# Performance work log

Measured on AMD Instinct MI355X. Metric: run time of the kernel, lower is better.

The kernel has to match this reference:

```python
import jax, jax.numpy as jnp
import numpy as np
from jax.scipy.ndimage import map_coordinates

IMG = 256
N_ANG = 50
BATCH = 4
N_CNN = 32
IN_CH = 2


def _circle_mask(S):
    c = (S - 1) / 2.0
    yy, xx = jnp.meshgrid(jnp.arange(S, dtype=jnp.float32), jnp.arange(S, dtype=jnp.float32), indexing='ij')
    return (((yy - c) ** 2 + (xx - c) ** 2) <= (S / 2.0) ** 2).astype(jnp.float32)


def radon_forward(img, angles):
    # img [B,1,S,S] -> sinogram [B,1,A,S]; parallel-beam, clip_to_circle=True
    S = img.shape[-1]
    c = (S - 1) / 2.0
    img = img * _circle_mask(S)
    t = jnp.arange(S, dtype=jnp.float32) - c        # integration coord
    s = jnp.arange(S, dtype=jnp.float32) - c        # detector coord
    cos = jnp.cos(angles)[:, None, None]
    sin = jnp.sin(angles)[:, None, None]
    x = s[None, None, :] * cos - t[None, :, None] * sin   # [A,S,S]
    y = s[None, None, :] * sin + t[None, :, None] * cos
    coords = jnp.stack([y + c, x + c])                    # [2,A,S,S] (row, col)
    samp = jax.vmap(lambda im: map_coordinates(im, coords, order=1, mode='constant', cval=0.0))(img[:, 0])  # [B,A,S,S]
    return samp.sum(axis=2)[:, None]                      # sum over ray param -> [B,1,A,S]


def filter_sinogram(sino):
    # Ram-Lak FFT filter with zero-padding + FBP normalization
    S = sino.shape[-1]
    A = sino.shape[2]
    P = max(64, int(2 ** np.ceil(np.log2(2 * S))))
    f = jnp.fft.rfft(jnp.pad(sino, ((0, 0), (0, 0), (0, 0), (0, P - S))), axis=-1)
    ramp = 2.0 * jnp.fft.rfftfreq(P).astype(jnp.float32)
    out = jnp.fft.irfft(f * ramp, n=P, axis=-1)[..., :S]
    return out * (np.pi / (2.0 * A))


def radon_backprojection(sino, angles):
    # sino [B,1,A,S] -> image [B,1,S,S]
    B, _, A, S = sino.shape
    c = (S - 1) / 2.0
    yy, xx = jnp.meshgrid(jnp.arange(S, dtype=jnp.float32) - c, jnp.arange(S, dtype=jnp.float32) - c, indexing='ij')
    cos = jnp.cos(angles)[:, None, None]
    sin = jnp.sin(angles)[:, None, None]
    det = xx[None] * cos + yy[None] * sin + c             # [A,S,S] detector coord
    sino2 = sino[:, 0]                                    # [B,A,S]

    def interp_one(sino_a, idx):
        # sino_a [B,S], idx [S,S] -> [B,S,S] linear interp, zero outside
        i0 = jnp.clip(jnp.floor(idx).astype(jnp.int32), 0, S - 2)
        w = idx - i0
        v = sino_a[:, i0] * (1.0 - w) + sino_a[:, i0 + 1] * w
        valid = (idx >= 0.0) & (idx <= S - 1.0)
        return jnp.where(valid, v, 0.0)

    bp = jax.vmap(interp_one, in_axes=(1, 0))(sino2, det).sum(axis=0)  # [B,S,S]
    return (bp * _circle_mask(S))[:, None]


def conv2d(x, w, b):
    y = jax.lax.conv_general_dilated(x, w, (1, 1), 'SAME', dimension_numbers=('NCHW', 'OIHW', 'NCHW'))
    return y + b[None, :, None, None]


def setup_inputs() -> dict:
    key = jax.random.key(0)
    ks = jax.random.split(key, 10)
    angles = jnp.asarray(np.linspace(0, np.pi, N_ANG, endpoint=False), dtype=jnp.float32)
    return {
        'x_sinogram': jax.random.normal(ks[0], (BATCH, 1, N_ANG, IMG), dtype=jnp.float32),
        'y_img_prev': jax.random.normal(ks[1], (BATCH, 1, IMG, IMG), dtype=jnp.float32),
        'y_img_concat_prev': jax.random.normal(ks[2], (BATCH, 1, IMG, IMG), dtype=jnp.float32),
        'angles': angles,
        'step': jnp.float32(1.0),
        'w1': jax.random.normal(ks[3], (N_CNN, IN_CH, 3, 3), dtype=jnp.float32) * 0.1,
        'b1': jnp.zeros((N_CNN,), dtype=jnp.float32),
        'w2': jax.random.normal(ks[4], (N_CNN, N_CNN, 3, 3), dtype=jnp.float32) * 0.1,
        'b2': jnp.zeros((N_CNN,), dtype=jnp.float32),
        'w3': jax.random.normal(ks[5], (1, N_CNN, 3, 3), dtype=jnp.float32) * 0.1,
        'b3': jnp.zeros((1,), dtype=jnp.float32),
    }


def reference(x_sinogram, y_img_prev, y_img_concat_prev, angles, step, w1, b1, w2, b2, w3, b3):
    Ay = radon_forward(y_img_prev, angles)                 # [B,1,A,S]
    diff = Ay - x_sinogram
    filt = filter_sinogram(diff)
    fbp = radon_backprojection(filt, angles)               # [B,1,S,S]
    y_img_update = y_img_prev + step * fbp
    y_cat = jnp.concatenate([y_img_update, y_img_concat_prev], axis=1)  # [B,2,S,S]
    h = jax.nn.relu(conv2d(y_cat, w1, b1))
    h = jax.nn.relu(conv2d(h, w2, b2))
    y_img = conv2d(h, w3, b3)
    return (y_img, y_img_update)
```

## Files before the change

kernel.cpp:

```cpp
#include <hip/hip_runtime.h>
#include <math.h>

#define IMGS 256
#define NANG 50
#define BATCH 4
#define NCNN 32
#define PIX (IMGS*IMGS)
#define NPIX (BATCH*PIX)

#define OFF_FILT  0
#define OFF_W2BF  51200

static constexpr double PI_D = 3.14159265358979323846;

typedef unsigned short u16;
typedef unsigned int   u32;
typedef unsigned long long u64;
typedef __bf16 bfrag __attribute__((ext_vector_type(8)));
typedef float  ffrag __attribute__((ext_vector_type(4)));

__device__ __forceinline__ u16 f2bf(float f) {
    u32 u = __float_as_uint(f);
    u += 0x7fffu + ((u >> 16) & 1u);
    return (u16)(u >> 16);
}

#define RPITCH_D 131
__global__ __launch_bounds__(1024, 4) void k_A(const float* __restrict__ angles,
                                               const float* __restrict__ yprev,
                                               const float* __restrict__ xsino,
                                               const float* __restrict__ w2,
                                               float* __restrict__ ws) {
    __shared__ u16 limg[258 * 262];
    __shared__ float spart[1024];
    __shared__ float staps[512];
    __shared__ float srow[256];
    int tid = threadIdx.x;
    int gid = blockIdx.x;
    if (gid >= 200) {
        int i = (gid - 200) * 1024 + tid;
        if (i < 9216) {
            int t = i >> 10, oc = (i >> 5) & 31, ic = i & 31;
            ((u16*)(ws + OFF_W2BF))[i] = f2bf(w2[(oc * 32 + ic) * 9 + t]);
        }
        return;
    }
    u32* l32 = (u32*)limg;
    int ra = gid;
    int a = ra % NANG, b = ra / NANG;

    if (tid < 511) {
        int d = tid - 255;
        int n = d < 0 ? -d : d;
        double g;
        if (n == 0) {
            g = 0.5;
        } else {
            double th = PI_D * (double)n / 256.0;
            double S = (256.0 * cos(255.0 * th) - 255.0 * cos(256.0 * th) - 1.0)
                       / (2.0 * (1.0 - cos(th)));
            double sign = (n & 1) ? -1.0 : 1.0;
            g = (sign + S / 128.0) / 512.0;
        }
        staps[tid] = (float)(g * PI_D / 100.0);
    }

    for (int z = tid; z < 772; z += 1024) {
        int addr;
        if (z < 258)      addr = z * RPITCH_D;
        else if (z < 516) addr = (z - 258) * RPITCH_D + 129;
        else if (z < 644) addr = (z - 516) + 1;
        else              addr = 257 * RPITCH_D + (z - 644) + 1;
        l32[addr] = 0;
    }
    const float* __restrict__ src = yprev + b * PIX;
    for (int idx = tid; idx < 16384; idx += 1024) {
        int r = idx >> 6, c4 = (idx & 63) << 2;
        float4 v = *(const float4*)(src + r * 256 + c4);
        float di = (float)r - 127.5f;
        float rr = di * di;
        float d0 = (float)c4 - 127.5f;
        v.x = (rr + d0 * d0 <= 16384.0f) ? v.x : 0.0f;
        v.y = (rr + (d0 + 1.0f) * (d0 + 1.0f) <= 16384.0f) ? v.y : 0.0f;
        v.z = (rr + (d0 + 2.0f) * (d0 + 2.0f) <= 16384.0f) ? v.z : 0.0f;
        v.w = (rr + (d0 + 3.0f) * (d0 + 3.0f) <= 16384.0f) ? v.w : 0.0f;
        u32 p0 = (u32)f2bf(v.x) | ((u32)f2bf(v.y) << 16);
        u32 p1 = (u32)f2bf(v.z) | ((u32)f2bf(v.w) << 16);
        int dw = (r + 1) * RPITCH_D + (c4 >> 1) + 1;
        l32[dw] = p0; l32[dw + 1] = p1;
    }
    __syncthreads();

    float a_ = angles[a];
    float cs = cosf(a_), sn = sinf(a_);
    int lane = tid & 63, w = tid >> 6;
    int s8 = lane & 7, t8 = lane >> 3;
    int sA = w * 16 + s8;
    float scA = (float)sA - 127.5f;

    float loA = (float)(w * 16) - 127.5f, hiA = loA + 7.0f;
    float loB = loA + 8.0f,               hiB = hiA + 8.0f;
    float s2minA = fminf(loA * loA, hiA * hiA);
    float s2maxA = fmaxf(loA * loA, hiA * hiA);
    float s2minB = fminf(loB * loB, hiB * hiB);
    float s2maxB = fmaxf(loB * loB, hiB * hiB);
    float s2min  = fminf(s2minA, s2minB);
    float s2max  = fmaxf(s2maxA, s2maxB);
    float hmax = sqrtf(16770.25f - s2min);
    int j_lo = max(0, (int)ceilf((120.5f - hmax) * 0.125f));
    int j_hi = min(31, (int)floorf((127.5f + hmax) * 0.125f));

    float tc0 = (float)t8 - 127.5f + 8.0f * (float)j_lo;
    float rowA = scA * sn + tc0 * cs + 127.5f;
    float colA = scA * cs - tc0 * sn + 127.5f;
    float rowB = rowA + 8.0f * sn;
    float colB = colA + 8.0f * cs;
    float cs8 = 8.0f * cs, sn8 = 8.0f * sn;
    float accA = 0.0f, accB = 0.0f;
    #pragma unroll 2
    for (int j = j_lo; j <= j_hi; ++j) {
        float t0j = 8.0f * (float)j - 127.5f;
        float t7j = t0j + 7.0f;
        float tmax2 = fmaxf(t0j * t0j, t7j * t7j);
        if (s2max + tmax2 <= 16384.0f) {
            #pragma unroll
            for (int hh = 0; hh < 2; ++hh) {
                float rowv = hh ? rowB : rowA;
                float colv = hh ? colB : colA;
                float fr = floorf(rowv), fc = floorf(colv);
                float wr = rowv - fr, wc = colv - fc;
                int i0 = (int)fr, j0 = (int)fc;
                int ca = j0 + 2;
                int ka = ca >> 1;
                int sh = (ca & 1) << 4;
                int dw = (i0 + 1) * RPITCH_D + ka;
                u32 A = l32[dw],            C = l32[dw + 1];
                u32 B = l32[dw + RPITCH_D], D = l32[dw + RPITCH_D + 1];
                u32 top = (u32)((((u64)C << 32) | (u64)A) >> sh);
                u32 bot = (u32)((((u64)D << 32) | (u64)B) >> sh);
                float tl = __uint_as_float(top << 16);
                float tr_ = __uint_as_float(top & 0xffff0000u);
                float bl = __uint_as_float(bot << 16);
                float br = __uint_as_float(bot & 0xffff0000u);
                float tv = tl + (tr_ - tl) * wc;
                float bv = bl + (br - bl) * wc;
                float sv = tv + (bv - tv) * wr;
                if (hh) accB += sv; else accA += sv;
            }
        } else {
            #pragma unroll
            for (int hh = 0; hh < 2; ++hh) {
                float rowv = hh ? rowB : rowA;
                float colv = hh ? colB : colA;
                float fr = floorf(rowv), fc = floorf(colv);
                float wr = rowv - fr, wc = colv - fc;
                int i0 = (int)fr, j0 = (int)fc;
                bool valid = (rowv > -1.0f) & (rowv < 256.0f) & (colv > -1.0f) & (colv < 256.0f);
                int i0c = min(max(i0, -1), 255);
                int j0c = min(max(j0, -1), 255);
                int ca = j0c + 2;
                int ka = ca >> 1;
                int sh = (ca & 1) << 4;
                int dw = (i0c + 1) * RPITCH_D + ka;
                u32 A = l32[dw],            C = l32[dw + 1];
                u32 B = l32[dw + RPITCH_D], D = l32[dw + RPITCH_D + 1];
                u32 top = (u32)((((u64)C << 32) | (u64)A) >> sh);
                u32 bot = (u32)((((u64)D << 32) | (u64)B) >> sh);
                float tl = __uint_as_float(top << 16);
                float tr_ = __uint_as_float(top & 0xffff0000u);
                float bl = __uint_as_float(bot << 16);
                float br = __uint_as_float(bot & 0xffff0000u);
                float tv = tl + (tr_ - tl) * wc;
                float bv = bl + (br - bl) * wc;
                float sv = tv + (bv - tv) * wr;
                sv = valid ? sv : 0.0f;
                if (hh) accB += sv; else accA += sv;
            }
        }
        rowA += cs8; colA -= sn8; rowB += cs8; colB -= sn8;
    }
    accA += __shfl_xor(accA, 8, 64);
    accA += __shfl_xor(accA, 16, 64);
    accA += __shfl_xor(accA, 32, 64);
    accB += __shfl_xor(accB, 8, 64);
    accB += __shfl_xor(accB, 16, 64);
    accB += __shfl_xor(accB, 32, 64);
    if (t8 == 0) { spart[sA] = accA; spart[sA + 8] = accB; }
    __syncthreads();
    if (tid < 256)
        srow[tid] = spart[tid] - xsino[ra * 256 + tid];
    __syncthreads();
    {
        int s = tid & 255, q = tid >> 8;
        float fa = 0.0f;
        int m0 = q * 64;
        #pragma unroll 8
        for (int m = m0; m < m0 + 64; ++m) fa += srow[m] * staps[s - m + 255];
        spart[tid] = fa;
    }
    __syncthreads();
    if (tid < 256)
        ws[OFF_FILT + ra * 256 + tid] =
            spart[tid] + spart[tid + 256] + spart[tid + 512] + spart[tid + 768];
}

#define H2PITCH 36
#define SM_SF    0
#define SM_H1    0
#define SM_H2    51200
#define SM_SUPD  125504
#define SM_SY2   133824
#define SM_SCS   142144
#define SM_SSN   142344
#define SM_SWP   142544
#define SM_TOTAL 143120
#define H1QSTRIDE (6*130*8)

__global__ __launch_bounds__(512, 2) void k_BC(const float* __restrict__ angles,
                                               const float* __restrict__ yprev,
                                               const float* __restrict__ yconc,
                                               const float* __restrict__ stepp,
                                               const float* __restrict__ w1,
                                               const float* __restrict__ b1,
                                               const float* __restrict__ b2,
                                               const float* __restrict__ w3,
                                               const float* __restrict__ b3,
                                               float* __restrict__ ws,
                                               float* __restrict__ dout) {
    __shared__ __align__(16) unsigned char smem[SM_TOTAL];
    float* sf   = (float*)(smem + SM_SF);
    u16*   h1q  = (u16*)(smem + SM_H1);
    u16*   sh2  = (u16*)(smem + SM_H2);
    u32*   l32c = (u32*)(smem + SM_H2);
    float (*supd)[260] = (float(*)[260])(smem + SM_SUPD);
    float (*sy2)[260]  = (float(*)[260])(smem + SM_SY2);
    float* scs = (float*)(smem + SM_SCS);
    float* ssn = (float*)(smem + SM_SSN);
    u32*   swp = (u32*)(smem + SM_SWP);

    int tid = threadIdx.x;
    int b = blockIdx.x >> 7, tile = blockIdx.x & 127;
    int y0 = tile << 1;

    {
        const float4* s4 = (const float4*)(ws + OFF_FILT + b * (NANG * 256));
        float4* d4 = (float4*)sf;
        for (int idx = tid; idx < NANG * 64; idx += 512) d4[idx] = s4[idx];
    }
    if (tid < NANG) {
        float a_ = angles[tid];
        scs[tid] = cosf(a_); ssn[tid] = sinf(a_);
    }
    if (tid < 144) {
        int t = tid >> 4, kd = tid & 15;
        swp[tid] = (u32)f2bf(w3[(2 * kd) * 9 + t]) | ((u32)f2bf(w3[(2 * kd + 1) * 9 + t]) << 16);
    }
    if (tid < 32) {
        int r = tid >> 2, c4 = tid & 3;
        supd[r][(c4 < 2) ? c4 : (c4 + 256)] = 0.0f;
    }
    for (int idx = tid; idx < 8 * 260; idx += 512) {
        int r = idx / 260, c = idx - r * 260;
        int iy = y0 - 3 + r, ix = c - 2;
        sy2[r][c] = ((unsigned)iy < 256u && (unsigned)ix < 256u)
                        ? yconc[b * PIX + iy * 256 + ix] : 0.0f;
    }
    __syncthreads();

    {
        int j = tid & 255, r0 = tid >> 8;
        float xx = (float)j - 127.5f;
        float yyb = (float)(y0 - 3 + r0) - 127.5f;
        float ac0 = 0.f, ac1 = 0.f, ac2 = 0.f, ac3 = 0.f;
        #pragma unroll 2
        for (int a = 0; a < NANG; ++a) {
            float cs = scs[a], sn = ssn[a];
            float d2 = sn + sn;
            float f0 = xx * cs + yyb * sn + 127.5f;
            float f1 = f0 + d2, f2 = f1 + d2, f3 = f2 + d2;
            #define BPSAMP(ff, accv) { \
                float fl = floorf(ff); int i0 = (int)fl; \
                i0 = min(max(i0, 0), 254); \
                float wq = ff - (float)i0; \
                float v = sf[a * 256 + i0] * (1.0f - wq) + sf[a * 256 + i0 + 1] * wq; \
                accv += (ff >= 0.0f && ff <= 255.0f) ? v : 0.0f; }
            BPSAMP(f0, ac0) BPSAMP(f1, ac1) BPSAMP(f2, ac2) BPSAMP(f3, ac3)
            #undef BPSAMP
        }
        float step = stepp[0];
        float accs[4] = {ac0, ac1, ac2, ac3};
        #pragma unroll
        for (int k = 0; k < 4; ++k) {
            int lr = r0 + 2 * k;
            int iy = y0 - 3 + lr;
            float val = 0.0f;
            if ((unsigned)iy < 256u) {
                float yy = (float)iy - 127.5f;
                float mk = (xx * xx + yy * yy <= 16384.0f) ? 1.0f : 0.0f;
                val = yprev[b * PIX + iy * 256 + j] + step * accs[k] * mk;
                if (iy >= y0 && iy <= y0 + 1)
                    dout[NPIX + b * PIX + iy * 256 + j] = val;
            }
            supd[lr][j + 2] = val;
        }
    }
    __syncthreads();

    if (tid < 144) {
        int r = tid / 36, rem = tid % 36;
        int col = (rem < 18) ? 0 : 257, dw = rem % 18;
        l32c[(r * 258 + col) * 18 + dw] = 0;
    }
    #pragma unroll
    for (int r = 0; r < 4; ++r) {
        int hy = y0 - 1 + r;
        if (hy < 0 || hy > 255)
            for (int idx = tid; idx < 258 * 18; idx += 512)
                l32c[r * 258 * 18 + idx] = 0;
    }

    const u16* __restrict__ w2bf = (const u16*)(ws + OFF_W2BF);
    int wv = tid >> 6, lane = tid & 63;
    int m = lane & 15, quad = lane >> 4;
    bfrag Bf[9][2];
    #pragma unroll
    for (int t = 0; t < 9; ++t) {
        const u16* wp = w2bf + t * 1024 + m * 32 + quad * 8;
        Bf[t][0] = *(const bfrag*)(wp);
        Bf[t][1] = *(const bfrag*)(wp + 16 * 32);
    }
    float bias0 = b2[m], bias1 = b2[m + 16];

    for (int xh = 0; xh < 2; ++xh) {
        {
            int oc0 = wv * 4, qq = wv >> 1, hh = wv & 1;
            float W[72];
            const float4* wsrc = (const float4*)(w1 + oc0 * 18);
            #pragma unroll
            for (int i = 0; i < 18; ++i) ((float4*)W)[i] = wsrc[i];
            float bb0 = b1[oc0], bb1 = b1[oc0 + 1], bb2 = b1[oc0 + 2], bb3 = b1[oc0 + 3];
            u16* hq = h1q + qq * H1QSTRIDE + hh * 4;
            for (int it = 0; it < 7; ++it) {
                int idx = it * 64 + lane;
                if (idx < 390) {
                    int lr = idx / 65, pp = idx - lr * 65;
                    int ir = y0 - 2 + lr;
                    int P = xh * 128 + 2 * pp - 1;
                    int cb = P + 1 + 2 - xh * 256;
                    int cgb = P + 1;
                    float a00 = bb0, a01 = bb1, a02 = bb2, a03 = bb3;
                    float a10 = bb0, a11 = bb1, a12 = bb2, a13 = bb3;
                    #pragma unroll
                    for (int ky = 0; ky < 3; ++ky) {
                        float2 ua = *(const float2*)&supd[lr + ky][cgb];
                        float2 ub = *(const float2*)&supd[lr + ky][cgb + 2];
                        float2 ca = *(const float2*)&sy2[lr + ky][cgb];
                        float2 cb2 = *(const float2*)&sy2[lr + ky][cgb + 2];
                        float u[4]  = {ua.x, ua.y, ub.x, ub.y};
                        float c6[4] = {ca.x, ca.y, cb2.x, cb2.y};
                        #pragma unroll
                        for (int kx = 0; kx < 3; ++kx) {
                            int t = ky * 3 + kx;
                            float u0 = u[kx],     c0 = c6[kx];
                            float u1 = u[kx + 1], c1 = c6[kx + 1];
                            a00 += u0 * W[t]      + c0 * W[9 + t];
                            a01 += u0 * W[18 + t] + c0 * W[27 + t];
                            a02 += u0 * W[36 + t] + c0 * W[45 + t];
                            a03 += u0 * W[54 + t] + c0 * W[63 + t];
                            a10 += u1 * W[t]      + c1 * W[9 + t];
                            a11 += u1 * W[18 + t] + c1 * W[27 + t];
                            a12 += u1 * W[36 + t] + c1 * W[45 + t];
                            a13 += u1 * W[54 + t] + c1 * W[63 + t];
                        }
                    }
                    bool rowOK = (unsigned)ir < 256u;
                    bool v0 = rowOK && ((unsigned)P < 256u);
                    bool v1 = rowOK && ((unsigned)(P + 1) < 256u);
                    u32 q00 = 0, q01 = 0, q10 = 0, q11 = 0;
                    if (v0) {
                        q00 = (u32)f2bf(fmaxf(a00, 0.f)) | ((u32)f2bf(fmaxf(a01, 0.f)) << 16);
                        q01 = (u32)f2bf(fmaxf(a02, 0.f)) | ((u32)f2bf(fmaxf(a03, 0.f)) << 16);
                    }
                    if (v1) {
                        q10 = (u32)f2bf(fmaxf(a10, 0.f)) | ((u32)f2bf(fmaxf(a11, 0.f)) << 16);
                        q11 = (u32)f2bf(fmaxf(a12, 0.f)) | ((u32)f2bf(fmaxf(a13, 0.f)) << 16);
                    }
                    int cl = 2 * pp;
                    u32* op0 = (u32*)(hq + (lr * 130 + cl) * 8);
                    u32* op1 = (u32*)(hq + (lr * 130 + cl + 1) * 8);
                    op0[0] = q00; op0[1] = q01;
                    op1[0] = q10; op1[1] = q11;
                }
            }
        }
        __syncthreads();

        {
            const u16* Abase = h1q + quad * H1QSTRIDE;
            #pragma unroll
            for (int k = 0; k < 4; ++k) {
                int tl = wv + (k << 3);
                int ridx = tl >> 3, xt8 = tl & 7;
                int hy = y0 - 1 + ridx;
                bool valid = (unsigned)hy < 256u;
                int clb = (xt8 << 4) + m;
                bfrag A0[3], A1[3];
                #pragma unroll
                for (int tx = 0; tx < 3; ++tx)
                    A0[tx] = *(const bfrag*)(Abase + ((ridx + 0) * 130 + clb + tx) * 8);
                #pragma unroll
                for (int tx = 0; tx < 3; ++tx)
                    A1[tx] = *(const bfrag*)(Abase + ((ridx + 1) * 130 + clb + tx) * 8);
                ffrag c0 = {0.f, 0.f, 0.f, 0.f}, c1 = {0.f, 0.f, 0.f, 0.f};
                #pragma unroll
                for (int tx = 0; tx < 3; ++tx) {
                    c0 = __builtin_amdgcn_mfma_f32_16x16x32_bf16(A0[tx], Bf[tx][0], c0, 0, 0, 0);
                    c1 = __builtin_amdgcn_mfma_f32_16x16x32_bf16(A0[tx], Bf[tx][1], c1, 0, 0, 0);
                }
                #pragma unroll
                for (int tx = 0; tx < 3; ++tx)
                    A0[tx] = *(const bfrag*)(Abase + ((ridx + 2) * 130 + clb + tx) * 8);
                #pragma unroll
                for (int tx = 0; tx < 3; ++tx) {
                    c0 = __builtin_amdgcn_mfma_f32_16x16x32_bf16(A1[tx], Bf[3 + tx][0], c0, 0, 0, 0);
                    c1 = __builtin_amdgcn_mfma_f32_16x16x32_bf16(A1[tx], Bf[3 + tx][1], c1, 0, 0, 0);
                }
                #pragma unroll
                for (int tx = 0; tx < 3; ++tx) {
                    c0 = __builtin_amdgcn_mfma_f32_16x16x32_bf16(A0[tx], Bf[6 + tx][0], c0, 0, 0, 0);
                    c1 = __builtin_amdgcn_mfma_f32_16x16x32_bf16(A0[tx], Bf[6 + tx][1], c1, 0, 0, 0);
                }
                if (valid) {
                    #pragma unroll
                    for (int r = 0; r < 4; ++r) {
                        int px = xh * 128 + (xt8 << 4) + quad * 4 + r;
                        u16* op = sh2 + (ridx * 258 + px + 1) * H2PITCH;
                        op[m]      = f2bf(fmaxf(c0[r] + bias0, 0.0f));
                        op[m + 16] = f2bf(fmaxf(c1[r] + bias1, 0.0f));
                    }
                }
            }
        }
        __syncthreads();
    }

    {
        int rr = tid >> 8, x = tid & 255;
        int oy = y0 + rr;
        float acc = b3[0];
        #pragma unroll
        for (int ky = 0; ky < 3; ++ky) {
            #pragma unroll
            for (int cx = 0; cx < 3; ++cx) {
                int t = ky * 3 + cx;
                const uint2* q2 = (const uint2*)(l32c + ((rr + ky) * 258 + x + cx) * 18);
                const uint2* w2p = (const uint2*)(swp + t * 16);
                #pragma unroll
                for (int kd = 0; kd < 8; ++kd) {
                    uint2 hv = q2[kd];
                    uint2 wvv = w2p[kd];
                    acc += __uint_as_float(hv.x << 16) * __uint_as_float(wvv.x << 16)
                         + __uint_as_float(hv.x & 0xffff0000u) * __uint_as_float(wvv.x & 0xffff0000u)
                         + __uint_as_float(hv.y << 16) * __uint_as_float(wvv.y << 16)
                         + __uint_as_float(hv.y & 0xffff0000u) * __uint_as_float(wvv.y & 0xffff0000u);
                }
            }
        }
        dout[b * PIX + oy * 256 + x] = acc;
    }
}

extern "C" void kernel_launch(void* const* d_in, const int* in_sizes, int n_in,
                              void* d_out, int out_size, void* d_ws, size_t ws_size,
                              hipStream_t stream) {
    const float* xsino  = (const float*)d_in[0];
    const float* yprev  = (const float*)d_in[1];
    const float* yconc  = (const float*)d_in[2];
    const float* angles = (const float*)d_in[3];
    const float* stepp  = (const float*)d_in[4];
    const float* w1 = (const float*)d_in[5];
    const float* b1 = (const float*)d_in[6];
    const float* w2 = (const float*)d_in[7];
    const float* b2 = (const float*)d_in[8];
    const float* w3 = (const float*)d_in[9];
    const float* b3 = (const float*)d_in[10];
    float* out = (float*)d_out;
    float* ws  = (float*)d_ws;

    k_A<<<209, 1024, 0, stream>>>(angles, yprev, xsino, w2, ws);
    k_BC<<<BATCH * 128, 512, 0, stream>>>(angles, yprev, yconc, stepp, w1, b1,
                                          b2, w3, b3, ws, out);
}
```

Baseline: 175.8 us.

## Split fused conv stage into four column quarters to halve shared memory

```diff
diff --git a/kernel.cpp b/kernel.cpp
--- a/kernel.cpp
+++ b/kernel.cpp
@@ -204,19 +204,20 @@
             spart[tid] + spart[tid + 256] + spart[tid + 512] + spart[tid + 768];
 }
 
+#define H1COLS 82
+#define H1PLANE (6*H1COLS*4)
+#define H2COLS 80
 #define H2PITCH 36
-#define SM_SF    0
 #define SM_H1    0
-#define SM_H2    51200
-#define SM_SUPD  125504
-#define SM_SY2   133824
-#define SM_SCS   142144
-#define SM_SSN   142344
-#define SM_SWP   142544
-#define SM_TOTAL 143120
-#define H1QSTRIDE (6*130*8)
-
-__global__ __launch_bounds__(512, 2) void k_BC(const float* __restrict__ angles,
+#define SM_H2    31488
+#define SM_SUPD  54528
+#define SM_SY2   62848
+#define SM_SCS   71168
+#define SM_SSN   71368
+#define SM_SWP   71568
+#define SM_TOTAL 72192
+
+__global__ __launch_bounds__(512, 4) void k_BC(const float* __restrict__ angles,
                                                const float* __restrict__ yprev,
                                                const float* __restrict__ yconc,
                                                const float* __restrict__ stepp,
@@ -228,10 +229,10 @@
                                                float* __restrict__ ws,
                                                float* __restrict__ dout) {
     __shared__ __align__(16) unsigned char smem[SM_TOTAL];
-    float* sf   = (float*)(smem + SM_SF);
-    u16*   h1q  = (u16*)(smem + SM_H1);
+    float* sf   = (float*)(smem);
+    u16*   h1   = (u16*)(smem + SM_H1);
     u16*   sh2  = (u16*)(smem + SM_H2);
-    u32*   l32c = (u32*)(smem + SM_H2);
+    u32*   l32h2= (u32*)(smem + SM_H2);
     float (*supd)[260] = (float(*)[260])(smem + SM_SUPD);
     float (*sy2)[260]  = (float(*)[260])(smem + SM_SY2);
     float* scs = (float*)(smem + SM_SCS);
@@ -306,48 +307,30 @@
     }
     __syncthreads();
 
-    if (tid < 144) {
-        int r = tid / 36, rem = tid % 36;
-        int col = (rem < 18) ? 0 : 257, dw = rem % 18;
-        l32c[(r * 258 + col) * 18 + dw] = 0;
-    }
-    #pragma unroll
-    for (int r = 0; r < 4; ++r) {
-        int hy = y0 - 1 + r;
-        if (hy < 0 || hy > 255)
-            for (int idx = tid; idx < 258 * 18; idx += 512)
-                l32c[r * 258 * 18 + idx] = 0;
-    }
-
-    const u16* __restrict__ w2bf = (const u16*)(ws + OFF_W2BF);
     int wv = tid >> 6, lane = tid & 63;
     int m = lane & 15, quad = lane >> 4;
-    bfrag Bf[9][2];
-    #pragma unroll
-    for (int t = 0; t < 9; ++t) {
-        const u16* wp = w2bf + t * 1024 + m * 32 + quad * 8;
-        Bf[t][0] = *(const bfrag*)(wp);
-        Bf[t][1] = *(const bfrag*)(wp + 16 * 32);
-    }
     float bias0 = b2[m], bias1 = b2[m + 16];
-
-    for (int xh = 0; xh < 2; ++xh) {
+    const u16* __restrict__ w2bf = (const u16*)(ws + OFF_W2BF);
+
+    for (int xq = 0; xq < 4; ++xq) {
+        int xbase = xq * 64;
         {
-            int oc0 = wv * 4, qq = wv >> 1, hh = wv & 1;
+            int oc0 = wv * 4;
             float W[72];
             const float4* wsrc = (const float4*)(w1 + oc0 * 18);
             #pragma unroll
             for (int i = 0; i < 18; ++i) ((float4*)W)[i] = wsrc[i];
             float bb0 = b1[oc0], bb1 = b1[oc0 + 1], bb2 = b1[oc0 + 2], bb3 = b1[oc0 + 3];
-            u16* hq = h1q + qq * H1QSTRIDE + hh * 4;
-            for (int it = 0; it < 7; ++it) {
+            u16* hp = h1 + wv * H1PLANE;
+            #pragma unroll
+            for (int it = 0; it < 4; ++it) {
                 int idx = it * 64 + lane;
-                if (idx < 390) {
-                    int lr = idx / 65, pp = idx - lr * 65;
+                if (idx < 246) {
+                    int lr = idx / 41, pp = idx - lr * 41;
+                    int P = xbase - 9 + 2 * pp;
                     int ir = y0 - 2 + lr;
-                    int P = xh * 128 + 2 * pp - 1;
-                    int cb = P + 1 + 2 - xh * 256;
                     int cgb = P + 1;
+                    cgb = min(max(cgb, 0), 256);
                     float a00 = bb0, a01 = bb1, a02 = bb2, a03 = bb3;
                     float a10 = bb0, a11 = bb1, a12 = bb2, a13 = bb3;
                     #pragma unroll
@@ -385,88 +368,105 @@
                         q10 = (u32)f2bf(fmaxf(a10, 0.f)) | ((u32)f2bf(fmaxf(a11, 0.f)) << 16);
                         q11 = (u32)f2bf(fmaxf(a12, 0.f)) | ((u32)f2bf(fmaxf(a13, 0.f)) << 16);
                     }
-                    int cl = 2 * pp;
-                    u32* op0 = (u32*)(hq + (lr * 130 + cl) * 8);
-                    u32* op1 = (u32*)(hq + (lr * 130 + cl + 1) * 8);
-                    op0[0] = q00; op0[1] = q01;
-                    op1[0] = q10; op1[1] = q11;
+                    uint4* op = (uint4*)(hp + (lr * H1COLS + 2 * pp) * 4);
+                    *op = make_uint4(q00, q01, q10, q11);
                 }
             }
         }
         __syncthreads();
 
         {
-            const u16* Abase = h1q + quad * H1QSTRIDE;
-            #pragma unroll
-            for (int k = 0; k < 4; ++k) {
+            bfrag Bf[9][2];
+            #pragma unroll
+            for (int t = 0; t < 9; ++t) {
+                const u16* wp = w2bf + t * 1024 + m * 32 + quad * 8;
+                Bf[t][0] = *(const bfrag*)(wp);
+                Bf[t][1] = *(const bfrag*)(wp + 16 * 32);
+            }
+            #pragma unroll
+            for (int k = 0; k < 3; ++k) {
                 int tl = wv + (k << 3);
-                int ridx = tl >> 3, xt8 = tl & 7;
-                int hy = y0 - 1 + ridx;
-                bool valid = (unsigned)hy < 256u;
-                int clb = (xt8 << 4) + m;
-                bfrag A0[3], A1[3];
+                if (tl < 20) {
+                    int ridx = tl / 5, pt = tl - ridx * 5;
+                    int hy = y0 - 1 + ridx;
+                    bool hyOK = (unsigned)hy < 256u;
+                    int Lb = 16 * pt + m;
+                    const u16* qp = h1 + quad * (2 * H1PLANE);
+                    #define LDF(row, L, dst) { \
+                        const u16* p0_ = qp + ((row) * H1COLS + (L)) * 4; \
+                        uint2 lo_ = *(const uint2*)p0_; \
+                        uint2 hi_ = *(const uint2*)(p0_ + H1PLANE); \
+                        ((uint2*)&dst)[0] = lo_; ((uint2*)&dst)[1] = hi_; }
+                    bfrag A0[3], A1[3];
+                    #pragma unroll
+                    for (int tx = 0; tx < 3; ++tx) LDF(ridx + 0, Lb + tx, A0[tx])
+                    #pragma unroll
+                    for (int tx = 0; tx < 3; ++tx) LDF(ridx + 1, Lb + tx, A1[tx])
+                    ffrag c0 = {0.f, 0.f, 0.f, 0.f}, c1 = {0.f, 0.f, 0.f, 0.f};
+                    #pragma unroll
+                    for (int tx = 0; tx < 3; ++tx) {
+                        c0 = __builtin_amdgcn_mfma_f32_16x16x32_bf16(A0[tx], Bf[tx][0], c0, 0, 0, 0);
+                        c1 = __builtin_amdgcn_mfma_f32_16x16x32_bf16(A0[tx], Bf[tx][1], c1, 0, 0, 0);
+                    }
+                    #pragma unroll
+                    for (int tx = 0; tx < 3; ++tx) LDF(ridx + 2, Lb + tx, A0[tx])
+                    #pragma unroll
+                    for (int tx = 0; tx < 3; ++tx) {
+                        c0 = __builtin_amdgcn_mfma_f32_16x16x32_bf16(A1[tx], Bf[3 + tx][0], c0, 0, 0, 0);
+                        c1 = __builtin_amdgcn_mfma_f32_16x16x32_bf16(A1[tx], Bf[3 + tx][1], c1, 0, 0, 0);
+                    }
+                    #pragma unroll
+                    for (int tx = 0; tx < 3; ++tx) {
+                        c0 = __builtin_amdgcn_mfma_f32_16x16x32_bf16(A0[tx], Bf[6 + tx][0], c0, 0, 0, 0);
+                        c1 = __builtin_amdgcn_mfma_f32_16x16x32_bf16(A0[tx], Bf[6 + tx][1], c1, 0, 0, 0);
+                    }
+                    #undef LDF
+                    #pragma unroll
+                    for (int r = 0; r < 4; ++r) {
+                        int pl = 16 * pt + quad * 4 + r;
+                        int pimg = xbase - 8 + pl;
+                        bool ok = hyOK && ((unsigned)pimg < 256u);
+                        float f0 = ok ? fmaxf(c0[r] + bias0, 0.0f) : 0.0f;
+                        float f1 = ok ? fmaxf(c1[r] + bias1, 0.0f) : 0.0f;
+                        u16* op = sh2 + (ridx * H2COLS + pl) * H2PITCH;
+                        op[m]      = f2bf(f0);
+                        op[m + 16] = f2bf(f1);
+                    }
+                }
+            }
+        }
+        __syncthreads();
+
+        {
+            int px_q = tid >> 2, g = tid & 3;
+            int xl = px_q & 63, rr = px_q >> 6;
+            int oy = y0 + rr;
+            float acc = (g == 0) ? b3[0] : 0.0f;
+            #pragma unroll
+            for (int ky = 0; ky < 3; ++ky) {
                 #pragma unroll
-                for (int tx = 0; tx < 3; ++tx)
-                    A0[tx] = *(const bfrag*)(Abase + ((ridx + 0) * 130 + clb + tx) * 8);
-                #pragma unroll
-                for (int tx = 0; tx < 3; ++tx)
-                    A1[tx] = *(const bfrag*)(Abase + ((ridx + 1) * 130 + clb + tx) * 8);
-                ffrag c0 = {0.f, 0.f, 0.f, 0.f}, c1 = {0.f, 0.f, 0.f, 0.f};
-                #pragma unroll
-                for (int tx = 0; tx < 3; ++tx) {
-                    c0 = __builtin_amdgcn_mfma_f32_16x16x32_bf16(A0[tx], Bf[tx][0], c0, 0, 0, 0);
-                    c1 = __builtin_amdgcn_mfma_f32_16x16x32_bf16(A0[tx], Bf[tx][1], c1, 0, 0, 0);
+                for (int cx = 0; cx < 3; ++cx) {
+                    int t = ky * 3 + cx;
+                    int pl = xl + cx + 7;
+                    const uint2* q2 = (const uint2*)(l32h2 + ((rr + ky) * H2COLS + pl) * 18 + g * 4);
+                    const uint2* wp = (const uint2*)(swp + t * 16 + g * 4);
+                    uint2 h0 = q2[0], h1v = q2[1];
+                    uint2 w0 = wp[0], w1v = wp[1];
+                    acc += __uint_as_float(h0.x << 16) * __uint_as_float(w0.x << 16)
+                         + __uint_as_float(h0.x & 0xffff0000u) * __uint_as_float(w0.x & 0xffff0000u)
+                         + __uint_as_float(h0.y << 16) * __uint_as_float(w0.y << 16)
+                         + __uint_as_float(h0.y & 0xffff0000u) * __uint_as_float(w0.y & 0xffff0000u)
+                         + __uint_as_float(h1v.x << 16) * __uint_as_float(w1v.x << 16)
+                         + __uint_as_float(h1v.x & 0xffff0000u) * __uint_as_float(w1v.x & 0xffff0000u)
+                         + __uint_as_float(h1v.y << 16) * __uint_as_float(w1v.y << 16)
+                         + __uint_as_float(h1v.y & 0xffff0000u) * __uint_as_float(w1v.y & 0xffff0000u);
                 }
-                #pragma unroll
-                for (int tx = 0; tx < 3; ++tx)
-                    A0[tx] = *(const bfrag*)(Abase + ((ridx + 2) * 130 + clb + tx) * 8);
-                #pragma unroll
-                for (int tx = 0; tx < 3; ++tx) {
-                    c0 = __builtin_amdgcn_mfma_f32_16x16x32_bf16(A1[tx], Bf[3 + tx][0], c0, 0, 0, 0);
-                    c1 = __builtin_amdgcn_mfma_f32_16x16x32_bf16(A1[tx], Bf[3 + tx][1], c1, 0, 0, 0);
-                }
-                #pragma unroll
-                for (int tx = 0; tx < 3; ++tx) {
-                    c0 = __builtin_amdgcn_mfma_f32_16x16x32_bf16(A0[tx], Bf[6 + tx][0], c0, 0, 0, 0);
-                    c1 = __builtin_amdgcn_mfma_f32_16x16x32_bf16(A0[tx], Bf[6 + tx][1], c1, 0, 0, 0);
-                }
-                if (valid) {
-                    #pragma unroll
-                    for (int r = 0; r < 4; ++r) {
-                        int px = xh * 128 + (xt8 << 4) + quad * 4 + r;
-                        u16* op = sh2 + (ridx * 258 + px + 1) * H2PITCH;
-                        op[m]      = f2bf(fmaxf(c0[r] + bias0, 0.0f));
-                        op[m + 16] = f2bf(fmaxf(c1[r] + bias1, 0.0f));
-                    }
-                }
-            }
-        }
-        __syncthreads();
-    }
-
-    {
-        int rr = tid >> 8, x = tid & 255;
-        int oy = y0 + rr;
-        float acc = b3[0];
-        #pragma unroll
-        for (int ky = 0; ky < 3; ++ky) {
-            #pragma unroll
-            for (int cx = 0; cx < 3; ++cx) {
-                int t = ky * 3 + cx;
-                const uint2* q2 = (const uint2*)(l32c + ((rr + ky) * 258 + x + cx) * 18);
-                const uint2* w2p = (const uint2*)(swp + t * 16);
-                #pragma unroll
-                for (int kd = 0; kd < 8; ++kd) {
-                    uint2 hv = q2[kd];
-                    uint2 wvv = w2p[kd];
-                    acc += __uint_as_float(hv.x << 16) * __uint_as_float(wvv.x << 16)
-                         + __uint_as_float(hv.x & 0xffff0000u) * __uint_as_float(wvv.x & 0xffff0000u)
-                         + __uint_as_float(hv.y << 16) * __uint_as_float(wvv.y << 16)
-                         + __uint_as_float(hv.y & 0xffff0000u) * __uint_as_float(wvv.y & 0xffff0000u);
-                }
-            }
-        }
-        dout[b * PIX + oy * 256 + x] = acc;
+            }
+            acc += __shfl_xor(acc, 1, 64);
+            acc += __shfl_xor(acc, 2, 64);
+            if (g == 0)
+                dout[b * PIX + oy * 256 + xbase + xl] = acc;
+        }
     }
 }
 
```

New measurement: 356.6 us. 103% more time.
